# Performance work log

Measured on AMD Instinct MI355X. Metric: run time of the kernel, lower is better.

Reference implementation:

```python
import jax, jax.numpy as jnp
import numpy as np

C = 128  # channel dim, forced equal to W by the reshape logic

def conv1x1(x, w, b):
    # 1x1 conv == per-pixel channel GEMM
    return jnp.einsum('bhwc,cd->bhwd', x, w) + b

def setup_inputs() -> dict:
    key = jax.random.key(0)
    ks = jax.random.split(key, 6)
    B, H, W = 8, 256, 128
    s = 1.0 / np.sqrt(C)
    return {
        'x': jax.random.normal(ks[0], (B, H, W, C), jnp.float32),
        'w_theta': jax.random.normal(ks[1], (C, C), jnp.float32) * s,
        'b_theta': jnp.zeros((C,), jnp.float32),
        'w_phi': jax.random.normal(ks[2], (C, C), jnp.float32) * s,
        'b_phi': jnp.zeros((C,), jnp.float32),
        'w_g': jax.random.normal(ks[3], (C, C), jnp.float32) * s,
        'b_g': jnp.zeros((C,), jnp.float32),
        'w_sc': jax.random.normal(ks[4], (C, C), jnp.float32) * s,
        'b_sc': jnp.zeros((C,), jnp.float32),
        'w_out': jax.random.normal(ks[5], (3 * C, C), jnp.float32) * (1.0 / np.sqrt(3 * C)),
        'b_out': jnp.zeros((C,), jnp.float32),
    }

def reference(x, w_theta, b_theta, w_phi, b_phi, w_g, b_g, w_sc, b_sc, w_out, b_out):
    B, H, W, Cc = x.shape  # W == Cc == 128 by construction
    f_theta = conv1x1(x, w_theta, b_theta)
    f_phi = conv1x1(x, w_phi, b_phi)
    f_g = conv1x1(x, w_g, b_g)
    # flatten (B,H) into batch of row-strips, each [W, C]
    ft = f_theta.reshape(B * H, W, Cc)
    fp = f_phi.reshape(B * H, W, Cc)
    fg = f_g.reshape(B * H, W, Cc)
    # horizontal: sigmoid(phi @ theta^T) -> [B*H, W, W] -> [B,H,W,C] (W==C)
    h_att = jax.nn.sigmoid(jnp.einsum('nwc,nvc->nwv', fp, ft)).reshape(B, H, W, Cc)
    horizontal_result = h_att * x
    # vertical: sigmoid(g^T @ phi) -> [B*H, C, C] -> [B,H,W,C]
    v_att = jax.nn.sigmoid(jnp.einsum('nwc,nwd->ncd', fg, fp)).reshape(B, H, W, Cc)
    vertical_result = v_att * x
    short_cut = conv1x1(x, w_sc, b_sc)
    cab = jnp.concatenate([horizontal_result, short_cut, vertical_result], axis=-1)
    return conv1x1(cab, w_out, b_out)
```

## Files before the change

### kernel.cpp

```cpp
#include <hip/hip_runtime.h>


typedef __bf16 bf16x8 __attribute__((ext_vector_type(8)));
typedef __bf16 bf16x4 __attribute__((ext_vector_type(4)));
typedef float f32x16 __attribute__((ext_vector_type(16)));

__device__ __forceinline__ int swz(int row, int cb) {
    return (row << 8) + (cb ^ ((row & 15) << 4));
}
__device__ __forceinline__ float sigm(float t) {
    return 1.0f / (1.0f + __expf(-t));
}
__device__ __forceinline__ void bar() {
    asm volatile("s_waitcnt lgkmcnt(0)" ::: "memory");
    __builtin_amdgcn_s_barrier();
    asm volatile("" ::: "memory");
}

__global__ void prep_combine(const float* __restrict__ w_sc,
                             const float* __restrict__ b_sc,
                             const float* __restrict__ w_out,
                             const float* __restrict__ b_out,
                             float* __restrict__ wsc2,
                             float* __restrict__ bout2) {
    int k = blockIdx.x;
    int n = threadIdx.x;
    float acc = 0.f;
    for (int c = 0; c < 128; ++c)
        acc += w_sc[k * 128 + c] * w_out[(128 + c) * 128 + n];
    wsc2[k * 128 + n] = acc;
    if (k == 0) {
        float b = b_out[n];
        for (int c = 0; c < 128; ++c)
            b += b_sc[c] * w_out[(128 + c) * 128 + n];
        bout2[n] = b;
    }
}

__global__ void prep_pack(const float* __restrict__ wth,
                          const float* __restrict__ wph,
                          const float* __restrict__ wg,
                          const float* __restrict__ wout,
                          const float* __restrict__ wsc2,
                          __bf16* __restrict__ packs) {
    int m = blockIdx.x;
    const float* src;
    int rowoff = 0;
    if (m == 0) src = wth;
    else if (m == 1) src = wph;
    else if (m == 2) src = wg;
    else if (m == 3) { src = wout; rowoff = 0; }
    else if (m == 4) { src = wout; rowoff = 256; }
    else src = wsc2;
    __bf16* dst = packs + m * 16384;
    for (int i = threadIdx.x; i < 16384; i += blockDim.x) {
        int j = i & 7;
        int lane = (i >> 3) & 63;
        int kk = (i >> 9) & 7;
        int nt = i >> 12;
        int k = kk * 16 + ((lane >> 5) << 3) + j;
        int n = nt * 32 + (lane & 31);
        dst[i] = (__bf16)(src[(rowoff + k) * 128 + n]);
    }
}

#define FPB 32768
#define FGT 98304

__global__ __launch_bounds__(1024, 1)
void cab_main(const float* __restrict__ x,
              const float* __restrict__ b_theta,
              const float* __restrict__ b_phi,
              const float* __restrict__ b_g,
              const __bf16* __restrict__ packs,
              const float* __restrict__ bout2,
              float* __restrict__ out,
              int nstrips, int spb) {
    __shared__ __align__(16) char lds[131072];

    const int tid = threadIdx.x;
    const int l   = tid & 63;
    const int wv  = tid >> 6;
    const int ct  = wv & 3;
    const int rt  = wv >> 2;
    const int ln  = l & 31;
    const int lh  = l >> 5;
    const int colg = ct * 32 + ln;
    const int m0   = rt * 32;

    const __bf16* pTH = packs;
    const __bf16* pPH = packs + 16384;
    const __bf16* pG  = packs + 2 * 16384;
    const __bf16* pO0 = packs + 3 * 16384;
    const __bf16* pO2 = packs + 4 * 16384;
    const __bf16* pS2 = packs + 5 * 16384;

    const float biasTH = b_theta[colg];
    const float biasPH = b_phi[colg];
    const float biasG  = b_g[colg];
    const float biasO  = bout2[colg];

    const int s0 = blockIdx.x * spb;
    if (s0 >= nstrips) return;
    const float4* x4 = (const float4*)x;

    const int srow = tid >> 5;
    const int scb  = (tid & 31) * 8;

    float4 pf[2];

    {
        long base = (long)s0 * 4096;
#pragma unroll
        for (int c = 0; c < 2; ++c) {
#pragma unroll
            for (int q = 0; q < 2; ++q) pf[q] = x4[base + (c * 2 + q) * 1024 + tid];
#pragma unroll
            for (int q = 0; q < 2; ++q) {
                int row = (c * 2 + q) * 32 + srow;
                bf16x4 v;
                v[0] = (__bf16)pf[q].x; v[1] = (__bf16)pf[q].y;
                v[2] = (__bf16)pf[q].z; v[3] = (__bf16)pf[q].w;
                *(bf16x4*)(lds + swz(row, scb)) = v;
            }
        }
    }
    bar();

    for (int it = 0; it < spb; ++it) {
        const int s = s0 + it;
        const int XBo  = (it & 1) ? 65536 : 0;
        const int FPTo = 65536 - XBo;
        f32x16 acc;

#pragma unroll
        for (int i = 0; i < 16; ++i) acc[i] = 0.f;
#pragma unroll 2
        for (int kk = 0; kk < 8; ++kk) {
            bf16x8 b = *(const bf16x8*)(pPH + (((ct * 8 + kk) * 64 + l) << 3));
            bf16x8 a = *(const bf16x8*)(lds + XBo + swz(m0 + ln, kk * 32 + lh * 16));
            acc = __builtin_amdgcn_mfma_f32_32x32x16_bf16(a, b, acc, 0, 0, 0);
        }
#pragma unroll
        for (int r = 0; r < 16; ++r) {
            int row = m0 + (r & 3) + ((r >> 2) << 3) + (lh << 2);
            *(__bf16*)(lds + FPB + swz(row, colg * 2)) = (__bf16)(acc[r] + biasPH);
        }
#pragma unroll
        for (int q = 0; q < 4; ++q) {
            int w0 = m0 + (q << 3) + (lh << 2);
            bf16x4 v;
#pragma unroll
            for (int e = 0; e < 4; ++e) v[e] = (__bf16)(acc[q * 4 + e] + biasPH);
            *(bf16x4*)(lds + FPTo + swz(colg, w0 * 2)) = v;
        }

#pragma unroll
        for (int i = 0; i < 16; ++i) acc[i] = 0.f;
#pragma unroll 2
        for (int kk = 0; kk < 8; ++kk) {
            bf16x8 b = *(const bf16x8*)(pG + (((ct * 8 + kk) * 64 + l) << 3));
            bf16x8 a = *(const bf16x8*)(lds + XBo + swz(m0 + ln, kk * 32 + lh * 16));
            acc = __builtin_amdgcn_mfma_f32_32x32x16_bf16(a, b, acc, 0, 0, 0);
        }
#pragma unroll
        for (int q = 0; q < 4; ++q) {
            int w0 = m0 + (q << 3) + (lh << 2);
            bf16x4 v;
#pragma unroll
            for (int e = 0; e < 4; ++e) v[e] = (__bf16)(acc[q * 4 + e] + biasG);
            *(bf16x4*)(lds + FGT + swz(colg, w0 * 2)) = v;
        }
        bar();

        if (it + 1 < spb) {
            long base = (long)(s + 1) * 4096;
#pragma unroll
            for (int q = 0; q < 2; ++q) pf[q] = x4[base + q * 1024 + tid];
        }

#pragma unroll
        for (int i = 0; i < 16; ++i) acc[i] = 0.f;
#pragma unroll 2
        for (int kk = 0; kk < 8; ++kk) {
            bf16x8 b = *(const bf16x8*)(lds + FGT + swz(colg, kk * 32 + lh * 16));
            bf16x8 a = *(const bf16x8*)(lds + FPTo + swz(m0 + ln, kk * 32 + lh * 16));
            acc = __builtin_amdgcn_mfma_f32_32x32x16_bf16(a, b, acc, 0, 0, 0);
        }
        bar();

#pragma unroll
        for (int q = 0; q < 4; ++q) {
            int j0 = m0 + (q << 3) + (lh << 2);
            bf16x4 xv = *(const bf16x4*)(lds + XBo + swz(colg, j0 * 2));
            bf16x4 v;
#pragma unroll
            for (int e = 0; e < 4; ++e)
                v[e] = (__bf16)(sigm(acc[q * 4 + e]) * (float)xv[e]);
            *(bf16x4*)(lds + FGT + swz(colg, j0 * 2)) = v;
        }

#pragma unroll
        for (int i = 0; i < 16; ++i) acc[i] = 0.f;
#pragma unroll 2
        for (int kk = 0; kk < 8; ++kk) {
            bf16x8 b = *(const bf16x8*)(pTH + (((ct * 8 + kk) * 64 + l) << 3));
            bf16x8 a = *(const bf16x8*)(lds + XBo + swz(m0 + ln, kk * 32 + lh * 16));
            acc = __builtin_amdgcn_mfma_f32_32x32x16_bf16(a, b, acc, 0, 0, 0);
        }
#pragma unroll
        for (int r = 0; r < 16; ++r) {
            int row = m0 + (r & 3) + ((r >> 2) << 3) + (lh << 2);
            *(__bf16*)(lds + FPTo + swz(row, colg * 2)) = (__bf16)(acc[r] + biasTH);
        }
        bar();

#pragma unroll
        for (int i = 0; i < 16; ++i) acc[i] = 0.f;
#pragma unroll 2
        for (int kk = 0; kk < 8; ++kk) {
            bf16x8 b = *(const bf16x8*)(lds + FPB + swz(colg, kk * 32 + lh * 16));
            bf16x8 a = *(const bf16x8*)(lds + FPTo + swz(m0 + ln, kk * 32 + lh * 16));
            acc = __builtin_amdgcn_mfma_f32_32x32x16_bf16(a, b, acc, 0, 0, 0);
        }
        bar();

        if (it + 1 < spb) {
#pragma unroll
            for (int q = 0; q < 2; ++q) {
                int row = q * 32 + srow;
                bf16x4 v;
                v[0] = (__bf16)pf[q].x; v[1] = (__bf16)pf[q].y;
                v[2] = (__bf16)pf[q].z; v[3] = (__bf16)pf[q].w;
                *(bf16x4*)(lds + FPTo + swz(row, scb)) = v;
            }
            long base = (long)(s + 1) * 4096;
#pragma unroll
            for (int q = 0; q < 2; ++q) pf[q] = x4[base + (2 + q) * 1024 + tid];
        }

#pragma unroll
        for (int q = 0; q < 4; ++q) {
            int v0 = m0 + (q << 3) + (lh << 2);
            bf16x4 xv = *(const bf16x4*)(lds + XBo + swz(colg, v0 * 2));
            bf16x4 v;
#pragma unroll
            for (int e = 0; e < 4; ++e)
                v[e] = (__bf16)(sigm(acc[q * 4 + e]) * (float)xv[e]);
            *(bf16x4*)(lds + FPB + swz(colg, v0 * 2)) = v;
        }
        bar();

#pragma unroll
        for (int i = 0; i < 16; ++i) acc[i] = 0.f;
#pragma unroll 2
        for (int kk = 0; kk < 8; ++kk) {
            bf16x8 b = *(const bf16x8*)(pO0 + (((ct * 8 + kk) * 64 + l) << 3));
            bf16x8 a = *(const bf16x8*)(lds + FPB + swz(m0 + ln, kk * 32 + lh * 16));
            acc = __builtin_amdgcn_mfma_f32_32x32x16_bf16(a, b, acc, 0, 0, 0);
        }
#pragma unroll 2
        for (int kk = 0; kk < 8; ++kk) {
            bf16x8 b = *(const bf16x8*)(pO2 + (((ct * 8 + kk) * 64 + l) << 3));
            bf16x8 a = *(const bf16x8*)(lds + FGT + swz(m0 + ln, kk * 32 + lh * 16));
            acc = __builtin_amdgcn_mfma_f32_32x32x16_bf16(a, b, acc, 0, 0, 0);
        }
#pragma unroll 2
        for (int kk = 0; kk < 8; ++kk) {
            bf16x8 b = *(const bf16x8*)(pS2 + (((ct * 8 + kk) * 64 + l) << 3));
            bf16x8 a = *(const bf16x8*)(lds + XBo + swz(m0 + ln, kk * 32 + lh * 16));
            acc = __builtin_amdgcn_mfma_f32_32x32x16_bf16(a, b, acc, 0, 0, 0);
        }
        {
            long obase = (long)s * 16384;
#pragma unroll
            for (int r = 0; r < 16; ++r) {
                int row = m0 + (r & 3) + ((r >> 2) << 3) + (lh << 2);
                out[obase + row * 128 + colg] = acc[r] + biasO;
            }
        }

        if (it + 1 < spb) {
#pragma unroll
            for (int q = 0; q < 2; ++q) {
                int row = 64 + q * 32 + srow;
                bf16x4 v;
                v[0] = (__bf16)pf[q].x; v[1] = (__bf16)pf[q].y;
                v[2] = (__bf16)pf[q].z; v[3] = (__bf16)pf[q].w;
                *(bf16x4*)(lds + FPTo + swz(row, scb)) = v;
            }
        }
        bar();
    }
}

extern "C" void kernel_launch(void* const* d_in, const int* in_sizes, int n_in,
                              void* d_out, int out_size, void* d_ws, size_t ws_size,
                              hipStream_t stream) {
    const float* x       = (const float*)d_in[0];
    const float* w_theta = (const float*)d_in[1];
    const float* b_theta = (const float*)d_in[2];
    const float* w_phi   = (const float*)d_in[3];
    const float* b_phi   = (const float*)d_in[4];
    const float* w_g     = (const float*)d_in[5];
    const float* b_g     = (const float*)d_in[6];
    const float* w_sc    = (const float*)d_in[7];
    const float* b_sc    = (const float*)d_in[8];
    const float* w_out   = (const float*)d_in[9];
    const float* b_out   = (const float*)d_in[10];
    float* out = (float*)d_out;

    float* wsc2 = (float*)d_ws;
    __bf16* packs = (__bf16*)((char*)d_ws + 65536);
    float* bout2 = (float*)((char*)d_ws + 65536 + 6 * 16384 * 2);

    int NS = in_sizes[0] / 16384;
    int spb = NS / 256;
    if (spb < 1) spb = 1;
    int grid = (NS + spb - 1) / spb;

    prep_combine<<<128, 128, 0, stream>>>(w_sc, b_sc, w_out, b_out, wsc2, bout2);
    prep_pack<<<6, 256, 0, stream>>>(w_theta, w_phi, w_g, w_out, wsc2, packs);
    cab_main<<<grid, 1024, 0, stream>>>(x, b_theta, b_phi, b_g, packs, bout2, out, NS, spb);
}
```

Measured before the change: 177.4 us.

## Grow LDS and fold theta projection into first phase to drop a barrier

Shared memory grows from 128 KB to 160 KB and is re-laid out. The x double buffer now sits at 0/32K, and phi-transposed, phi and g get dedicated regions. Because of this the theta projection can be computed in the first phase alongside the phi and g projections, writing into the non-current x buffer. That removes one block-wide barrier per strip iteration and merges two GEMM phases. The cost is more LDS per block, which must fit the device limit, and more work before the first barrier.

```diff
diff --git a/kernel.cpp b/kernel.cpp
--- a/kernel.cpp
+++ b/kernel.cpp
@@ -64,8 +64,9 @@
     }
 }
 
-#define FPB 32768
-#define FGT 98304
+#define FPBo 65536
+#define FPTo 98304
+#define FGTo 131072
 
 __global__ __launch_bounds__(1024, 1)
 void cab_main(const float* __restrict__ x,
@@ -76,7 +77,7 @@
               const float* __restrict__ bout2,
               float* __restrict__ out,
               int nstrips, int spb) {
-    __shared__ __align__(16) char lds[131072];
+    __shared__ __align__(16) char lds[163840];
 
     const int tid = threadIdx.x;
     const int l   = tid & 63;
@@ -129,8 +130,8 @@
 
     for (int it = 0; it < spb; ++it) {
         const int s = s0 + it;
-        const int XBo  = (it & 1) ? 65536 : 0;
-        const int FPTo = 65536 - XBo;
+        const int XBo  = (it & 1) ? 32768 : 0;
+        const int FTBo = 32768 - XBo;
         f32x16 acc;
 
 #pragma unroll
@@ -144,7 +145,7 @@
 #pragma unroll
         for (int r = 0; r < 16; ++r) {
             int row = m0 + (r & 3) + ((r >> 2) << 3) + (lh << 2);
-            *(__bf16*)(lds + FPB + swz(row, colg * 2)) = (__bf16)(acc[r] + biasPH);
+            *(__bf16*)(lds + FPBo + swz(row, colg * 2)) = (__bf16)(acc[r] + biasPH);
         }
 #pragma unroll
         for (int q = 0; q < 4; ++q) {
@@ -169,7 +170,21 @@
             bf16x4 v;
 #pragma unroll
             for (int e = 0; e < 4; ++e) v[e] = (__bf16)(acc[q * 4 + e] + biasG);
-            *(bf16x4*)(lds + FGT + swz(colg, w0 * 2)) = v;
+            *(bf16x4*)(lds + FGTo + swz(colg, w0 * 2)) = v;
+        }
+
+#pragma unroll
+        for (int i = 0; i < 16; ++i) acc[i] = 0.f;
+#pragma unroll 2
+        for (int kk = 0; kk < 8; ++kk) {
+            bf16x8 b = *(const bf16x8*)(pTH + (((ct * 8 + kk) * 64 + l) << 3));
+            bf16x8 a = *(const bf16x8*)(lds + XBo + swz(m0 + ln, kk * 32 + lh * 16));
+            acc = __builtin_amdgcn_mfma_f32_32x32x16_bf16(a, b, acc, 0, 0, 0);
+        }
+#pragma unroll
+        for (int r = 0; r < 16; ++r) {
+            int row = m0 + (r & 3) + ((r >> 2) << 3) + (lh << 2);
+            *(__bf16*)(lds + FTBo + swz(row, colg * 2)) = (__bf16)(acc[r] + biasTH);
         }
         bar();
 
@@ -183,7 +198,7 @@
         for (int i = 0; i < 16; ++i) acc[i] = 0.f;
 #pragma unroll 2
         for (int kk = 0; kk < 8; ++kk) {
-            bf16x8 b = *(const bf16x8*)(lds + FGT + swz(colg, kk * 32 + lh * 16));
+            bf16x8 b = *(const bf16x8*)(lds + FGTo + swz(colg, kk * 32 + lh * 16));
             bf16x8 a = *(const bf16x8*)(lds + FPTo + swz(m0 + ln, kk * 32 + lh * 16));
             acc = __builtin_amdgcn_mfma_f32_32x32x16_bf16(a, b, acc, 0, 0, 0);
         }
@@ -197,30 +212,15 @@
 #pragma unroll
             for (int e = 0; e < 4; ++e)
                 v[e] = (__bf16)(sigm(acc[q * 4 + e]) * (float)xv[e]);
-            *(bf16x4*)(lds + FGT + swz(colg, j0 * 2)) = v;
-        }
-
-#pragma unroll
-        for (int i = 0; i < 16; ++i) acc[i] = 0.f;
-#pragma unroll 2
-        for (int kk = 0; kk < 8; ++kk) {
-            bf16x8 b = *(const bf16x8*)(pTH + (((ct * 8 + kk) * 64 + l) << 3));
-            bf16x8 a = *(const bf16x8*)(lds + XBo + swz(m0 + ln, kk * 32 + lh * 16));
-            acc = __builtin_amdgcn_mfma_f32_32x32x16_bf16(a, b, acc, 0, 0, 0);
-        }
-#pragma unroll
-        for (int r = 0; r < 16; ++r) {
-            int row = m0 + (r & 3) + ((r >> 2) << 3) + (lh << 2);
-            *(__bf16*)(lds + FPTo + swz(row, colg * 2)) = (__bf16)(acc[r] + biasTH);
-        }
-        bar();
-
-#pragma unroll
-        for (int i = 0; i < 16; ++i) acc[i] = 0.f;
-#pragma unroll 2
-        for (int kk = 0; kk < 8; ++kk) {
-            bf16x8 b = *(const bf16x8*)(lds + FPB + swz(colg, kk * 32 + lh * 16));
-            bf16x8 a = *(const bf16x8*)(lds + FPTo + swz(m0 + ln, kk * 32 + lh * 16));
+            *(bf16x4*)(lds + FGTo + swz(colg, j0 * 2)) = v;
+        }
+
+#pragma unroll
+        for (int i = 0; i < 16; ++i) acc[i] = 0.f;
+#pragma unroll 2
+        for (int kk = 0; kk < 8; ++kk) {
+            bf16x8 b = *(const bf16x8*)(lds + FPBo + swz(colg, kk * 32 + lh * 16));
+            bf16x8 a = *(const bf16x8*)(lds + FTBo + swz(m0 + ln, kk * 32 + lh * 16));
             acc = __builtin_amdgcn_mfma_f32_32x32x16_bf16(a, b, acc, 0, 0, 0);
         }
         bar();
@@ -232,7 +232,7 @@
                 bf16x4 v;
                 v[0] = (__bf16)pf[q].x; v[1] = (__bf16)pf[q].y;
                 v[2] = (__bf16)pf[q].z; v[3] = (__bf16)pf[q].w;
-                *(bf16x4*)(lds + FPTo + swz(row, scb)) = v;
+                *(bf16x4*)(lds + FTBo + swz(row, scb)) = v;
             }
             long base = (long)(s + 1) * 4096;
 #pragma unroll
@@ -247,7 +247,7 @@
 #pragma unroll
             for (int e = 0; e < 4; ++e)
                 v[e] = (__bf16)(sigm(acc[q * 4 + e]) * (float)xv[e]);
-            *(bf16x4*)(lds + FPB + swz(colg, v0 * 2)) = v;
+            *(bf16x4*)(lds + FPBo + swz(colg, v0 * 2)) = v;
         }
         bar();
 
@@ -256,13 +256,13 @@
 #pragma unroll 2
         for (int kk = 0; kk < 8; ++kk) {
             bf16x8 b = *(const bf16x8*)(pO0 + (((ct * 8 + kk) * 64 + l) << 3));
-            bf16x8 a = *(const bf16x8*)(lds + FPB + swz(m0 + ln, kk * 32 + lh * 16));
+            bf16x8 a = *(const bf16x8*)(lds + FPBo + swz(m0 + ln, kk * 32 + lh * 16));
             acc = __builtin_amdgcn_mfma_f32_32x32x16_bf16(a, b, acc, 0, 0, 0);
         }
 #pragma unroll 2
         for (int kk = 0; kk < 8; ++kk) {
             bf16x8 b = *(const bf16x8*)(pO2 + (((ct * 8 + kk) * 64 + l) << 3));
-            bf16x8 a = *(const bf16x8*)(lds + FGT + swz(m0 + ln, kk * 32 + lh * 16));
+            bf16x8 a = *(const bf16x8*)(lds + FGTo + swz(m0 + ln, kk * 32 + lh * 16));
             acc = __builtin_amdgcn_mfma_f32_32x32x16_bf16(a, b, acc, 0, 0, 0);
         }
 #pragma unroll 2
@@ -287,7 +287,7 @@
                 bf16x4 v;
                 v[0] = (__bf16)pf[q].x; v[1] = (__bf16)pf[q].y;
                 v[2] = (__bf16)pf[q].z; v[3] = (__bf16)pf[q].w;
-                *(bf16x4*)(lds + FPTo + swz(row, scb)) = v;
+                *(bf16x4*)(lds + FTBo + swz(row, scb)) = v;
             }
         }
         bar();
```

New measurement: 242.6 us. +36.7%, slower.
